# Performance work log

Measured on AMD Instinct MI355X. Metric: run time of the kernel, lower is better.

Reference implementation:

```python
import jax, jax.numpy as jnp
import numpy as np

INPUT_DIM = 1024
LATENT_DIM = 100
NUM_EMBEDDINGS = 21
COMMITMENT_COST = 0.1
BATCH = 65536


def setup_inputs() -> dict:
    key = jax.random.key(0)
    k_x, k_we, k_be, k_cb, k_wd, k_bd = jax.random.split(key, 6)
    x = jax.random.normal(k_x, (BATCH, INPUT_DIM), dtype=jnp.float32)
    # nn.Linear default init ~ U(-1/sqrt(fan_in), 1/sqrt(fan_in)); approx with scaled uniform
    s_e = 1.0 / np.sqrt(INPUT_DIM)
    W_enc = jax.random.uniform(k_we, (LATENT_DIM, INPUT_DIM), jnp.float32, -s_e, s_e)
    b_enc = jax.random.uniform(k_be, (LATENT_DIM,), jnp.float32, -s_e, s_e)
    # codebook init ~ U(-1/num_embeddings, 1/num_embeddings)
    s_c = 1.0 / NUM_EMBEDDINGS
    codebook = jax.random.uniform(k_cb, (NUM_EMBEDDINGS, LATENT_DIM), jnp.float32, -s_c, s_c)
    s_d = 1.0 / np.sqrt(LATENT_DIM)
    W_dec = jax.random.uniform(k_wd, (INPUT_DIM, LATENT_DIM), jnp.float32, -s_d, s_d)
    b_dec = jax.random.uniform(k_bd, (INPUT_DIM,), jnp.float32, -s_d, s_d)
    return {"x": x, "W_enc": W_enc, "b_enc": b_enc, "codebook": codebook,
            "W_dec": W_dec, "b_dec": b_dec}


def reference(x, W_enc, b_enc, codebook, W_dec, b_dec):
    # Encoder: (B, D_in) -> (B, L)
    z_e = x @ W_enc.T + b_enc
    # Squared L2 distances to codebook: (B, K)
    distances = (jnp.sum(z_e ** 2, axis=-1, keepdims=True)
                 + jnp.sum(codebook ** 2, axis=1)[None, :]
                 - 2.0 * (z_e @ codebook.T))
    encoding_indices = jnp.argmin(distances, axis=-1, keepdims=True)  # (B, 1) int
    z_q = codebook[encoding_indices[:, 0]]  # (B, L)
    sg = jax.lax.stop_gradient
    vq_loss = (jnp.mean((sg(z_q) - z_e) ** 2)
               + COMMITMENT_COST * jnp.mean((sg(z_e) - z_q) ** 2))
    # Straight-through estimator
    z_q_st = z_e + sg(z_q - z_e)
    # Decoder: (B, L) -> (B, D_in)
    x_recon = z_q_st @ W_dec.T + b_dec
    return (x_recon, vq_loss, encoding_indices)
```

## Files before the change

kernel.cpp:

```cpp
#include <hip/hip_runtime.h>
#include <hip/hip_bf16.h>

#define BATCH   65536
#define D       1024
#define L       100
#define C       21
#define NPAD    112

typedef __bf16 bf16x8 __attribute__((ext_vector_type(8)));
typedef float  f32x4  __attribute__((ext_vector_type(4)));

static constexpr size_t OFF_P  = 8192;
static constexpr size_t OFF_U  = OFF_P + (size_t)BATCH * 4;
static constexpr size_t OFF_T  = OFF_U + (size_t)C * D * 4;
static constexpr size_t OFF_R  = OFF_T + 128;
static constexpr size_t OFF_WB = OFF_R + (size_t)C * D * 4;

__global__ __launch_bounds__(256) void k_setup(
    const float* __restrict__ W_enc, const float* __restrict__ b_enc,
    const float* __restrict__ cb,    const float* __restrict__ W_dec,
    const float* __restrict__ b_dec,
    float* __restrict__ u, float* __restrict__ t, float* __restrict__ R,
    __bf16* __restrict__ Wb)
{
    int id = blockIdx.x * 256 + threadIdx.x;
    if (id < C * D) {
        int c = id >> 10, k = id & 1023;
        float s = 0.f;
        for (int j = 0; j < L; j++) s += cb[c * L + j] * W_enc[j * D + k];
        u[id] = s;
    } else if (id < 2 * C * D) {
        int i2 = id - C * D;
        int c = i2 >> 10, k = i2 & 1023;
        float s = 0.f;
        for (int j = 0; j < L; j++) s += cb[c * L + j] * W_dec[k * L + j];
        R[i2] = s + b_dec[k];
    } else if (id < 2 * C * D + NPAD * D) {
        int i3 = id - 2 * C * D;
        int n = i3 >> 10, k = i3 & 1023;
        Wb[i3] = (n < L) ? (__bf16)W_enc[n * D + k] : (__bf16)0.f;
    } else if (id < 2 * C * D + NPAD * D + C) {
        int c = id - 2 * C * D - NPAD * D;
        float s = 0.f, b2 = 0.f;
        for (int j = 0; j < L; j++) {
            float cv = cb[c * L + j];
            s  += cv * cv;
            b2 += b_enc[j] * cv;
        }
        t[c] = s - 2.f * b2;
    }
}

__global__ __launch_bounds__(256) void k_score(
    const float* __restrict__ x, const float* __restrict__ u,
    const float* __restrict__ t, const float* __restrict__ R,
    float* __restrict__ outR, float* __restrict__ outIdx,
    float* __restrict__ p)
{
    __shared__ float part[4][64][24];
    __shared__ int   idxs[64];

    const int lane = threadIdx.x & 63;
    const int wave = __builtin_amdgcn_readfirstlane(threadIdx.x >> 6);
    const int row0 = blockIdx.x * 64;
    const int row  = row0 + lane;

    float acc[C];
#pragma unroll
    for (int c = 0; c < C; c++) acc[c] = 0.f;

    const float4* xr = (const float4*)(x + (size_t)row * D + wave * 256);
    const float*  ub = u + wave * 256;

    for (int k4 = 0; k4 < 64; k4++) {
        float4 xv = xr[k4];
#pragma unroll
        for (int c = 0; c < C; c++) {
            const float* uc = ub + c * D + k4 * 4;
            acc[c] += xv.x * uc[0] + xv.y * uc[1] + xv.z * uc[2] + xv.w * uc[3];
        }
    }
#pragma unroll
    for (int c = 0; c < C; c++) part[wave][lane][c] = acc[c];
    __syncthreads();

    if (wave == 0) {
        float best = 3.0e38f;
        int   bi   = 0;
#pragma unroll
        for (int c = 0; c < C; c++) {
            float s = part[0][lane][c] + part[1][lane][c]
                    + part[2][lane][c] + part[3][lane][c];
            float score = t[c] - 2.0f * s;
            if (score < best) { best = score; bi = c; }
        }
        idxs[lane]   = bi;
        p[row]       = best;
        outIdx[row]  = (float)bi;
    }
    __syncthreads();

    for (int r = 0; r < 64; r++) {
        int id = idxs[r];
        float4 v = ((const float4*)(R + (size_t)id * D))[threadIdx.x];
        ((float4*)(outR + (size_t)(row0 + r) * D))[threadIdx.x] = v;
    }
}

__global__ __launch_bounds__(256) void k_loss(
    const float* __restrict__ x, const __bf16* __restrict__ Wb,
    const float* __restrict__ b_enc, const float* __restrict__ p,
    double* __restrict__ bsums)
{
    __shared__ float bpart[16];

    const int lane = threadIdx.x & 63;
    const int wave = __builtin_amdgcn_readfirstlane(threadIdx.x >> 6);
    const int n15  = lane & 15;
    const int q    = lane >> 4;
    const int m16  = blockIdx.x * 64 + wave * 16;

    f32x4 acc[7];
#pragma unroll
    for (int nt = 0; nt < 7; nt++) acc[nt] = (f32x4){0.f, 0.f, 0.f, 0.f};

    const float* xrow = x + (size_t)(m16 + n15) * D + q * 8;

    for (int k0 = 0; k0 < D; k0 += 32) {
        float4 a0 = *(const float4*)(xrow + k0);
        float4 a1 = *(const float4*)(xrow + k0 + 4);
        bf16x8 af;
        af[0] = (__bf16)a0.x; af[1] = (__bf16)a0.y; af[2] = (__bf16)a0.z; af[3] = (__bf16)a0.w;
        af[4] = (__bf16)a1.x; af[5] = (__bf16)a1.y; af[6] = (__bf16)a1.z; af[7] = (__bf16)a1.w;
#pragma unroll
        for (int nt = 0; nt < 7; nt++) {
            bf16x8 bfr = *(const bf16x8*)(Wb + (size_t)(nt * 16 + n15) * D + k0 + q * 8);
            acc[nt] = __builtin_amdgcn_mfma_f32_16x16x32_bf16(af, bfr, acc[nt], 0, 0, 0);
        }
    }

    float rn[4] = {0.f, 0.f, 0.f, 0.f};
#pragma unroll
    for (int nt = 0; nt < 7; nt++) {
        int col = nt * 16 + n15;
        float bn = (col < L) ? b_enc[col] : 0.f;
#pragma unroll
        for (int r = 0; r < 4; r++) {
            float z = acc[nt][r] + bn;
            rn[r] += z * z;
        }
    }
#pragma unroll
    for (int off = 1; off < 16; off <<= 1) {
#pragma unroll
        for (int r = 0; r < 4; r++) rn[r] += __shfl_xor(rn[r], off, 64);
    }

    if (n15 == 0) {
        float s4 = 0.f;
#pragma unroll
        for (int r = 0; r < 4; r++) s4 += rn[r] + p[m16 + q * 4 + r];
        bpart[wave * 4 + q] = s4;
    }
    __syncthreads();
    if (threadIdx.x == 0) {
        double bs = 0.0;
        for (int i = 0; i < 16; i++) bs += (double)bpart[i];
        bsums[blockIdx.x] = bs;
    }
}

__global__ __launch_bounds__(256) void k_final(
    const double* __restrict__ bsums, float* __restrict__ out_loss)
{
    __shared__ double wsum[4];
    int t = threadIdx.x;
    double s = bsums[t] + bsums[t + 256] + bsums[t + 512] + bsums[t + 768];
    for (int off = 32; off; off >>= 1) s += __shfl_down(s, off, 64);
    if ((t & 63) == 0) wsum[t >> 6] = s;
    __syncthreads();
    if (t == 0) {
        double tot = wsum[0] + wsum[1] + wsum[2] + wsum[3];
        out_loss[0] = (float)(1.1 * tot / ((double)BATCH * (double)L));
    }
}

extern "C" void kernel_launch(void* const* d_in, const int* in_sizes, int n_in,
                              void* d_out, int out_size, void* d_ws, size_t ws_size,
                              hipStream_t stream) {
    const float* x     = (const float*)d_in[0];
    const float* W_enc = (const float*)d_in[1];
    const float* b_enc = (const float*)d_in[2];
    const float* cb    = (const float*)d_in[3];
    const float* W_dec = (const float*)d_in[4];
    const float* b_dec = (const float*)d_in[5];

    char*   ws    = (char*)d_ws;
    double* bsums = (double*)ws;
    float*  p     = (float*)(ws + OFF_P);
    float*  u     = (float*)(ws + OFF_U);
    float*  t     = (float*)(ws + OFF_T);
    float*  R     = (float*)(ws + OFF_R);
    __bf16* Wb    = (__bf16*)(ws + OFF_WB);

    float* outR    = (float*)d_out;
    float* outLoss = outR + (size_t)BATCH * D;
    float* outIdx  = outLoss + 1;

    k_setup<<<617, 256, 0, stream>>>(W_enc, b_enc, cb, W_dec, b_dec, u, t, R, Wb);
    k_score<<<BATCH / 64, 256, 0, stream>>>(x, u, t, R, outR, outIdx, p);
    k_loss <<<BATCH / 64, 256, 0, stream>>>(x, Wb, b_enc, p, bsums);
    k_final<<<1, 256, 0, stream>>>(bsums, outLoss);
}
```

Before: 664.7 us.

## Fuse score and loss kernels into one pass over x

Merges the scoring kernel and the MFMA-based loss kernel into a single kernel, so x (256 MB) is read from memory once instead of twice. The score loop is re-tiled so each wave covers interleaved 16-column chunks across the full K range, in step with the MFMA loop, and a barrier in each iteration keeps the waves' loads aligned for cache reuse. The per-row best scores move from a global buffer into shared memory, and output rows are written with nontemporal stores. The cost is higher register pressure from holding both accumulator sets and extra barriers inside the loop.

```diff
diff --git a/kernel.cpp b/kernel.cpp
--- a/kernel.cpp
+++ b/kernel.cpp
@@ -51,39 +51,64 @@
     }
 }
 
-__global__ __launch_bounds__(256) void k_score(
+__global__ __launch_bounds__(256) void k_main(
     const float* __restrict__ x, const float* __restrict__ u,
     const float* __restrict__ t, const float* __restrict__ R,
+    const __bf16* __restrict__ Wb, const float* __restrict__ b_enc,
     float* __restrict__ outR, float* __restrict__ outIdx,
-    float* __restrict__ p)
+    double* __restrict__ bsums)
 {
-    __shared__ float part[4][64][24];
+    __shared__ float part[4][64][22];
+    __shared__ float pbest[64];
     __shared__ int   idxs[64];
+    __shared__ float bpart[16];
 
     const int lane = threadIdx.x & 63;
     const int wave = __builtin_amdgcn_readfirstlane(threadIdx.x >> 6);
     const int row0 = blockIdx.x * 64;
-    const int row  = row0 + lane;
-
-    float acc[C];
-#pragma unroll
-    for (int c = 0; c < C; c++) acc[c] = 0.f;
-
-    const float4* xr = (const float4*)(x + (size_t)row * D + wave * 256);
-    const float*  ub = u + wave * 256;
-
-    for (int k4 = 0; k4 < 64; k4++) {
-        float4 xv = xr[k4];
-#pragma unroll
-        for (int c = 0; c < C; c++) {
-            const float* uc = ub + c * D + k4 * 4;
-            acc[c] += xv.x * uc[0] + xv.y * uc[1] + xv.z * uc[2] + xv.w * uc[3];
-        }
-    }
-#pragma unroll
-    for (int c = 0; c < C; c++) part[wave][lane][c] = acc[c];
-    __syncthreads();
-
+    const int n15  = lane & 15;
+    const int q    = lane >> 4;
+
+    float sacc[C];
+#pragma unroll
+    for (int c = 0; c < C; c++) sacc[c] = 0.f;
+    f32x4 zacc[7];
+#pragma unroll
+    for (int nt = 0; nt < 7; nt++) zacc[nt] = (f32x4){0.f, 0.f, 0.f, 0.f};
+
+    const float* xs = x + (size_t)(row0 + lane) * D + wave * 16;
+    const float* ub = u + wave * 16;
+    const float* xm = x + (size_t)(row0 + wave * 16 + n15) * D + q * 8;
+
+    for (int k0 = 0; k0 < D; k0 += 64) {
+#pragma unroll
+        for (int j2 = 0; j2 < 4; j2++) {
+            float4 xv = *(const float4*)(xs + k0 + j2 * 4);
+#pragma unroll
+            for (int c = 0; c < C; c++) {
+                const float* uc = ub + c * D + k0 + j2 * 4;
+                sacc[c] += xv.x * uc[0] + xv.y * uc[1] + xv.z * uc[2] + xv.w * uc[3];
+            }
+        }
+#pragma unroll
+        for (int ks = 0; ks < 2; ks++) {
+            float4 a0 = *(const float4*)(xm + k0 + ks * 32);
+            float4 a1 = *(const float4*)(xm + k0 + ks * 32 + 4);
+            bf16x8 af;
+            af[0] = (__bf16)a0.x; af[1] = (__bf16)a0.y; af[2] = (__bf16)a0.z; af[3] = (__bf16)a0.w;
+            af[4] = (__bf16)a1.x; af[5] = (__bf16)a1.y; af[6] = (__bf16)a1.z; af[7] = (__bf16)a1.w;
+#pragma unroll
+            for (int nt = 0; nt < 7; nt++) {
+                bf16x8 bfr = *(const bf16x8*)(Wb + (size_t)(nt * 16 + n15) * D + k0 + ks * 32 + q * 8);
+                zacc[nt] = __builtin_amdgcn_mfma_f32_16x16x32_bf16(af, bfr, zacc[nt], 0, 0, 0);
+            }
+        }
+        __builtin_amdgcn_s_barrier();
+    }
+
+#pragma unroll
+    for (int c = 0; c < C; c++) part[wave][lane][c] = sacc[c];
+    __syncthreads();
     if (wave == 0) {
         float best = 3.0e38f;
         int   bi   = 0;
@@ -94,50 +119,11 @@
             float score = t[c] - 2.0f * s;
             if (score < best) { best = score; bi = c; }
         }
-        idxs[lane]   = bi;
-        p[row]       = best;
-        outIdx[row]  = (float)bi;
-    }
-    __syncthreads();
-
-    for (int r = 0; r < 64; r++) {
-        int id = idxs[r];
-        float4 v = ((const float4*)(R + (size_t)id * D))[threadIdx.x];
-        ((float4*)(outR + (size_t)(row0 + r) * D))[threadIdx.x] = v;
-    }
-}
-
-__global__ __launch_bounds__(256) void k_loss(
-    const float* __restrict__ x, const __bf16* __restrict__ Wb,
-    const float* __restrict__ b_enc, const float* __restrict__ p,
-    double* __restrict__ bsums)
-{
-    __shared__ float bpart[16];
-
-    const int lane = threadIdx.x & 63;
-    const int wave = __builtin_amdgcn_readfirstlane(threadIdx.x >> 6);
-    const int n15  = lane & 15;
-    const int q    = lane >> 4;
-    const int m16  = blockIdx.x * 64 + wave * 16;
-
-    f32x4 acc[7];
-#pragma unroll
-    for (int nt = 0; nt < 7; nt++) acc[nt] = (f32x4){0.f, 0.f, 0.f, 0.f};
-
-    const float* xrow = x + (size_t)(m16 + n15) * D + q * 8;
-
-    for (int k0 = 0; k0 < D; k0 += 32) {
-        float4 a0 = *(const float4*)(xrow + k0);
-        float4 a1 = *(const float4*)(xrow + k0 + 4);
-        bf16x8 af;
-        af[0] = (__bf16)a0.x; af[1] = (__bf16)a0.y; af[2] = (__bf16)a0.z; af[3] = (__bf16)a0.w;
-        af[4] = (__bf16)a1.x; af[5] = (__bf16)a1.y; af[6] = (__bf16)a1.z; af[7] = (__bf16)a1.w;
-#pragma unroll
-        for (int nt = 0; nt < 7; nt++) {
-            bf16x8 bfr = *(const bf16x8*)(Wb + (size_t)(nt * 16 + n15) * D + k0 + q * 8);
-            acc[nt] = __builtin_amdgcn_mfma_f32_16x16x32_bf16(af, bfr, acc[nt], 0, 0, 0);
-        }
-    }
+        idxs[lane]         = bi;
+        pbest[lane]        = best;
+        outIdx[row0 + lane] = (float)bi;
+    }
+    __syncthreads();
 
     float rn[4] = {0.f, 0.f, 0.f, 0.f};
 #pragma unroll
@@ -146,7 +132,7 @@
         float bn = (col < L) ? b_enc[col] : 0.f;
 #pragma unroll
         for (int r = 0; r < 4; r++) {
-            float z = acc[nt][r] + bn;
+            float z = zacc[nt][r] + bn;
             rn[r] += z * z;
         }
     }
@@ -155,11 +141,10 @@
 #pragma unroll
         for (int r = 0; r < 4; r++) rn[r] += __shfl_xor(rn[r], off, 64);
     }
-
     if (n15 == 0) {
         float s4 = 0.f;
 #pragma unroll
-        for (int r = 0; r < 4; r++) s4 += rn[r] + p[m16 + q * 4 + r];
+        for (int r = 0; r < 4; r++) s4 += rn[r] + pbest[wave * 16 + q * 4 + r];
         bpart[wave * 4 + q] = s4;
     }
     __syncthreads();
@@ -167,6 +152,12 @@
         double bs = 0.0;
         for (int i = 0; i < 16; i++) bs += (double)bpart[i];
         bsums[blockIdx.x] = bs;
+    }
+
+    for (int r = 0; r < 64; r++) {
+        int id = idxs[r];
+        const f32x4 v = ((const f32x4*)(R + (size_t)id * D))[threadIdx.x];
+        __builtin_nontemporal_store(v, ((f32x4*)(outR + (size_t)(row0 + r) * D)) + threadIdx.x);
     }
 }
 
@@ -197,7 +188,6 @@
 
     char*   ws    = (char*)d_ws;
     double* bsums = (double*)ws;
-    float*  p     = (float*)(ws + OFF_P);
     float*  u     = (float*)(ws + OFF_U);
     float*  t     = (float*)(ws + OFF_T);
     float*  R     = (float*)(ws + OFF_R);
@@ -208,7 +198,6 @@
     float* outIdx  = outLoss + 1;
 
     k_setup<<<617, 256, 0, stream>>>(W_enc, b_enc, cb, W_dec, b_dec, u, t, R, Wb);
-    k_score<<<BATCH / 64, 256, 0, stream>>>(x, u, t, R, outR, outIdx, p);
-    k_loss <<<BATCH / 64, 256, 0, stream>>>(x, Wb, b_enc, p, bsums);
+    k_main <<<BATCH / 64, 256, 0, stream>>>(x, u, t, R, Wb, b_enc, outR, outIdx, bsums);
     k_final<<<1, 256, 0, stream>>>(bsums, outLoss);
 }
```

New measurement: 564.4 us. -15.1%, faster.
